# Kernel optimization log

Measured on AMD Instinct MI355X. Metric: run time of the kernel, lower is better.

The kernel has to match this reference:

```python
import jax, jax.numpy as jnp
import numpy as np
from jax import lax

UP = 2
K = 3
IN_C, OUT_C = 64, 64
PAD = K // 2  # 1
WEIGHT_GAIN = 1.0 / np.sqrt(IN_C * K * K)
ACT_GAIN = np.sqrt(2.0)  # lrelu def_gain
CLAMP = 256.0
LRELU_ALPHA = 0.2


def setup_inputs() -> dict:
    key = jax.random.key(0)
    k1, k2 = jax.random.split(key)
    x = jax.random.normal(k1, (16, IN_C, 128, 128), dtype=jnp.float32)
    weight = jax.random.normal(k2, (OUT_C, IN_C, K, K), dtype=jnp.float32)
    bias = jnp.zeros((OUT_C,), dtype=jnp.float32)
    # upfirdn2d.setup_filter((1,3,3,1)): outer product, normalized to sum 1
    a = jnp.array([1.0, 3.0, 3.0, 1.0], dtype=jnp.float32)
    f = jnp.outer(a, a)
    f = f / jnp.sum(f)  # 4x4 separable FIR filter
    return {"x": x, "weight": weight, "bias": bias, "f": f}


def _upfirdn2d_up2(x, f):
    # zero-insertion upsample by 2 + pad + FIR filter, gain = up**2
    N, C, H, W = x.shape
    fw = f.shape[-1]  # 4
    # conv2d_resample padding adjustment for up>1 on top of base padding k//2
    p0 = PAD + (fw + UP - 1) // 2  # 3
    p1 = PAD + (fw - UP) // 2      # 2
    fk = jnp.tile((f * (UP * UP))[None, None], (C, 1, 1, 1))  # [C,1,4,4] depthwise
    # lhs_dilation=2 gives 2H-1 samples; add (UP-1) extra right/bottom zeros to
    # match upfirdn's 2H zero-inserted signal.
    return lax.conv_general_dilated(
        x, fk, window_strides=(1, 1),
        padding=((p0, p1 + UP - 1), (p0, p1 + UP - 1)),
        lhs_dilation=(UP, UP),
        feature_group_count=C,
        dimension_numbers=("NCHW", "OIHW", "NCHW"))


def reference(x, weight, bias, f):
    h = _upfirdn2d_up2(x, f)  # [N, C, 2H+2, 2W+2]
    # conv: flip_weight = (up == 1) = False -> true convolution (flip kernel)
    w = (weight * WEIGHT_GAIN)[:, :, ::-1, ::-1]
    y = lax.conv_general_dilated(
        h, w, window_strides=(1, 1), padding="VALID",
        dimension_numbers=("NCHW", "OIHW", "NCHW"))  # [N, OUT_C, 2H, 2W]
    # fused bias + lrelu + gain + clamp (bias_act with gain=1)
    y = y + bias[None, :, None, None]
    y = jnp.where(y >= 0, y, LRELU_ALPHA * y) * ACT_GAIN
    y = jnp.clip(y, -CLAMP, CLAMP)
    return y
```

## Files before the change

kernel.cpp:

```cpp
#include <hip/hip_runtime.h>

typedef float f32x16 __attribute__((ext_vector_type(16)));
typedef float f32x4  __attribute__((ext_vector_type(4)));
typedef float f32x2  __attribute__((ext_vector_type(2)));
typedef short bf16x8 __attribute__((ext_vector_type(8)));

#define NB 16
#define CI 64
#define CO 64
#define Hh 128
#define Ww 128

__device__ short g_A[9 * 4 * 8 * 64 * 8];
__device__ short g_xh[(size_t)NB * Hh * Ww * CI];

__device__ inline short f2bf(float f) {
  union { float f; unsigned u; } v; v.f = f;
  unsigned r = (v.u + 0x7FFF + ((v.u >> 16) & 1)) >> 16;
  return (short)r;
}

__global__ __launch_bounds__(256) void build_filters(const float* __restrict__ w) {
  const int ef = blockIdx.x * 256 + threadIdx.x;
  if (ef >= 147456) return;
  const int e   = ef & 7;
  const int l   = (ef >> 3) & 63;
  const int mg  = (ef >> 9) & 7;
  const int ks  = (ef >> 12) & 3;
  const int tap = ef >> 14;
  const int r   = l & 31;
  const int px  = r & 1;
  const int py  = mg >> 2;
  const int oc  = (mg & 3) * 16 + (r >> 1);
  const int ic  = ks * 16 + (l >> 5) * 8 + e;
  const int dyi = tap / 3, dxi = tap % 3;
  const int my = 2 * dyi + 1 - py;
  const int mx = 2 * dxi + 1 - px;
  const float FF[4] = {0.25f, 0.75f, 0.75f, 0.25f};
  const float* wp = w + (oc * CI + ic) * 9;
  float s = 0.f;
  #pragma unroll
  for (int ky = 0; ky < 3; ++ky) {
    const int iy = my - ky;
    if (iy < 0 || iy > 3) continue;
    #pragma unroll
    for (int kx = 0; kx < 3; ++kx) {
      const int ix = mx - kx;
      if (ix < 0 || ix > 3) continue;
      s += wp[(2 - ky) * 3 + (2 - kx)] * (FF[iy] * FF[ix]);
    }
  }
  g_A[ef] = f2bf(s * (1.0f / 24.0f));
}

__global__ __launch_bounds__(256) void to_nhwc(const float* __restrict__ x) {
  __shared__ alignas(16) char xt[64 * 512];
  const int b = blockIdx.x;
  const int n = b >> 7, y = b & 127;
  const int tid = threadIdx.x;
  #pragma unroll
  for (int it = 0; it < 8; ++it) {
    const int idx = tid + it * 256;
    const int ic = idx >> 5, xq = idx & 31;
    const f32x4 v = *(const f32x4*)(x + (((size_t)n * CI + ic) * Hh + y) * Ww + xq * 4);
    *(f32x4*)(xt + ic * 512 + ((xq * 16) ^ (((ic >> 3) & 7) * 16))) = v;
  }
  __syncthreads();
  #pragma unroll
  for (int it = 0; it < 4; ++it) {
    const int idx = tid + it * 256;
    const int icb = idx & 7, xp = idx >> 3;
    bf16x8 o;
    #pragma unroll
    for (int j = 0; j < 8; ++j) {
      const int ic = icb * 8 + j;
      const float f = *(const float*)(xt + ic * 512 + (((xp >> 2) * 16) ^ (icb * 16)) + (xp & 3) * 4);
      o[j] = f2bf(f);
    }
    *(bf16x8*)(g_xh + (((size_t)n * Hh + y) * Ww + xp) * CI + icb * 8) = o;
  }
}

#define CH_STR 2896

__global__ __launch_bounds__(256, 2) void mfma_conv(const float* __restrict__ bias,
                                                    float* __restrict__ out) {
  __shared__ alignas(16) char xs[8 * CH_STR];

  const int tid = threadIdx.x;
  const int l   = tid & 63;
  const int wid = tid >> 6;
  const int wm  = wid >> 1;
  const int wn  = wid & 1;
  const int n   = blockIdx.y;
  const int ty0 = blockIdx.x >> 3, tx0 = blockIdx.x & 7;
  const int qb  = ty0 * 8, pb = tx0 * 16;

  bf16x8 a[4][4];
  #pragma unroll
  for (int ks = 0; ks < 4; ++ks)
    #pragma unroll
    for (int mf = 0; mf < 4; ++mf)
      a[ks][mf] = *(const bf16x8*)(g_A + ((ks * 8 + wm * 4 + mf) * 512) + l * 8);

  const size_t xbase = (size_t)n * (Hh * Ww * CI);
  for (int u = tid; u < 1440; u += 256) {
    const int icb8 = u & 7, pix = u >> 3;
    const int yy = pix / 18, xx = pix - yy * 18;
    const int gy = qb - 1 + yy, gx = pb - 1 + xx;
    bf16x8 v = {};
    if ((unsigned)gy < (unsigned)Hh && (unsigned)gx < (unsigned)Ww)
      v = *(const bf16x8*)(g_xh + xbase + (size_t)(gy * Ww + gx) * CI + icb8 * 8);
    *(bf16x8*)(xs + icb8 * CH_STR + pix * 16) = v;
  }
  __syncthreads();

  f32x16 acc[4][2];
  #pragma unroll
  for (int mf = 0; mf < 4; ++mf)
    #pragma unroll
    for (int nf = 0; nf < 2; ++nf)
      #pragma unroll
      for (int r = 0; r < 16; ++r) acc[mf][nf][r] = 0.f;

  const int col = l & 31, kg2 = l >> 5;
  const int p = col & 15, qh = col >> 4;
  int bbase[2];
  #pragma unroll
  for (int nf = 0; nf < 2; ++nf)
    bbase[nf] = kg2 * CH_STR + ((wn * 4 + nf * 2 + qh) * 18 + p) * 16;

  #pragma unroll
  for (int tap = 0; tap < 9; ++tap) {
    const int dyi = tap / 3, dxi = tap % 3;
    const int bsh = (dyi * 18 + dxi) * 16;
    #pragma unroll
    for (int ks = 0; ks < 4; ++ks) {
      bf16x8 b[2];
      #pragma unroll
      for (int nf = 0; nf < 2; ++nf)
        b[nf] = *(const bf16x8*)(xs + bbase[nf] + ks * (2 * CH_STR) + bsh);
      __builtin_amdgcn_s_setprio(1);
      #pragma unroll
      for (int mf = 0; mf < 4; ++mf)
        #pragma unroll
        for (int nf = 0; nf < 2; ++nf)
          acc[mf][nf] = __builtin_amdgcn_mfma_f32_32x32x16_bf16(a[ks][mf], b[nf], acc[mf][nf], 0, 0, 0);
      __builtin_amdgcn_s_setprio(0);
      if (tap < 8) {
        #pragma unroll
        for (int mf = 0; mf < 4; ++mf)
          a[ks][mf] = *(const bf16x8*)(g_A + (((tap + 1) * 4 + ks) * 8 + wm * 4 + mf) * 512 + l * 8);
      }
    }
  }

  float* outp = out + ((size_t)(n * CO) << 16);
  #pragma unroll
  for (int mf = 0; mf < 4; ++mf) {
    #pragma unroll
    for (int nf = 0; nf < 2; ++nf) {
      const int q = wn * 4 + nf * 2 + qh;
      const int y = 2 * (qb + q) + wm;
      const int xd = 2 * (pb + p);
      #pragma unroll
      for (int rp = 0; rp < 8; ++rp) {
        const int oc = mf * 16 + (rp & 1) + 4 * (rp >> 1) + 2 * kg2;
        const float bj = bias[oc];
        float v0 = acc[mf][nf][2 * rp]     + bj;
        float v1 = acc[mf][nf][2 * rp + 1] + bj;
        v0 = (v0 >= 0.f ? v0 : 0.2f * v0) * 1.4142135623730951f;
        v1 = (v1 >= 0.f ? v1 : 0.2f * v1) * 1.4142135623730951f;
        v0 = fminf(256.f, fmaxf(-256.f, v0));
        v1 = fminf(256.f, fmaxf(-256.f, v1));
        f32x2 o; o[0] = v0; o[1] = v1;
        __builtin_nontemporal_store(o, (f32x2*)(outp + ((size_t)oc << 16) + y * 256 + xd));
      }
    }
  }
}

extern "C" void kernel_launch(void* const* d_in, const int* in_sizes, int n_in,
                              void* d_out, int out_size, void* d_ws, size_t ws_size,
                              hipStream_t stream) {
  const float* x    = (const float*)d_in[0];
  const float* w    = (const float*)d_in[1];
  const float* bias = (const float*)d_in[2];
  float* out = (float*)d_out;

  build_filters<<<576, 256, 0, stream>>>(w);
  to_nhwc<<<2048, 256, 0, stream>>>(x);
  mfma_conv<<<dim3(128, NB), 256, 0, stream>>>(bias, out);
}
```

Measured before the change: 115.5 us.

## Merge prep kernels and halve conv tile height for higher occupancy

Folds the filter-building and NHWC-conversion kernels into one launch, with extra blocks handling the weights. The conv kernel's tile shrinks from 8 to 4 low-res rows, each wave now owning all pixels of its 2 M-fragments. The grid doubles, accumulator and A registers halve, LDS shrinks, and launch bounds ask for 3 blocks per SM. The cost is more halo reloading per output and less reuse of A fragments across pixels.

```diff
diff --git a/kernel.cpp b/kernel.cpp
--- a/kernel.cpp
+++ b/kernel.cpp
@@ -20,44 +20,48 @@
   return (short)r;
 }
 
-__global__ __launch_bounds__(256) void build_filters(const float* __restrict__ w) {
-  const int ef = blockIdx.x * 256 + threadIdx.x;
-  if (ef >= 147456) return;
-  const int e   = ef & 7;
-  const int l   = (ef >> 3) & 63;
-  const int mg  = (ef >> 9) & 7;
-  const int ks  = (ef >> 12) & 3;
-  const int tap = ef >> 14;
-  const int r   = l & 31;
-  const int px  = r & 1;
-  const int py  = mg >> 2;
-  const int oc  = (mg & 3) * 16 + (r >> 1);
-  const int ic  = ks * 16 + (l >> 5) * 8 + e;
-  const int dyi = tap / 3, dxi = tap % 3;
-  const int my = 2 * dyi + 1 - py;
-  const int mx = 2 * dxi + 1 - px;
-  const float FF[4] = {0.25f, 0.75f, 0.75f, 0.25f};
-  const float* wp = w + (oc * CI + ic) * 9;
-  float s = 0.f;
-  #pragma unroll
-  for (int ky = 0; ky < 3; ++ky) {
-    const int iy = my - ky;
-    if (iy < 0 || iy > 3) continue;
+__global__ __launch_bounds__(256) void prep(const float* __restrict__ x,
+                                            const float* __restrict__ w) {
+  const int tid = threadIdx.x;
+  if (blockIdx.x >= 2048) {
+    const int base = (blockIdx.x - 2048) * 2304;
     #pragma unroll
-    for (int kx = 0; kx < 3; ++kx) {
-      const int ix = mx - kx;
-      if (ix < 0 || ix > 3) continue;
-      s += wp[(2 - ky) * 3 + (2 - kx)] * (FF[iy] * FF[ix]);
+    for (int i = 0; i < 9; ++i) {
+      const int ef = base + i * 256 + tid;
+      const int e   = ef & 7;
+      const int l   = (ef >> 3) & 63;
+      const int mg  = (ef >> 9) & 7;
+      const int ks  = (ef >> 12) & 3;
+      const int tap = ef >> 14;
+      const int r   = l & 31;
+      const int px  = r & 1;
+      const int py  = mg >> 2;
+      const int oc  = (mg & 3) * 16 + (r >> 1);
+      const int ic  = ks * 16 + (l >> 5) * 8 + e;
+      const int dyi = tap / 3, dxi = tap % 3;
+      const int my = 2 * dyi + 1 - py;
+      const int mx = 2 * dxi + 1 - px;
+      const float FF[4] = {0.25f, 0.75f, 0.75f, 0.25f};
+      const float* wp = w + (oc * CI + ic) * 9;
+      float s = 0.f;
+      #pragma unroll
+      for (int ky = 0; ky < 3; ++ky) {
+        const int iy = my - ky;
+        if (iy < 0 || iy > 3) continue;
+        #pragma unroll
+        for (int kx = 0; kx < 3; ++kx) {
+          const int ix = mx - kx;
+          if (ix < 0 || ix > 3) continue;
+          s += wp[(2 - ky) * 3 + (2 - kx)] * (FF[iy] * FF[ix]);
+        }
+      }
+      g_A[ef] = f2bf(s * (1.0f / 24.0f));
     }
+    return;
   }
-  g_A[ef] = f2bf(s * (1.0f / 24.0f));
-}
-
-__global__ __launch_bounds__(256) void to_nhwc(const float* __restrict__ x) {
   __shared__ alignas(16) char xt[64 * 512];
   const int b = blockIdx.x;
   const int n = b >> 7, y = b & 127;
-  const int tid = threadIdx.x;
   #pragma unroll
   for (int it = 0; it < 8; ++it) {
     const int idx = tid + it * 256;
@@ -81,30 +85,28 @@
   }
 }
 
-#define CH_STR 2896
+#define CH_STR 1728
 
-__global__ __launch_bounds__(256, 2) void mfma_conv(const float* __restrict__ bias,
+__global__ __launch_bounds__(256, 3) void mfma_conv(const float* __restrict__ bias,
                                                     float* __restrict__ out) {
   __shared__ alignas(16) char xs[8 * CH_STR];
 
   const int tid = threadIdx.x;
   const int l   = tid & 63;
   const int wid = tid >> 6;
-  const int wm  = wid >> 1;
-  const int wn  = wid & 1;
   const int n   = blockIdx.y;
   const int ty0 = blockIdx.x >> 3, tx0 = blockIdx.x & 7;
-  const int qb  = ty0 * 8, pb = tx0 * 16;
+  const int qb  = ty0 * 4, pb = tx0 * 16;
 
-  bf16x8 a[4][4];
+  bf16x8 a[4][2];
   #pragma unroll
   for (int ks = 0; ks < 4; ++ks)
     #pragma unroll
-    for (int mf = 0; mf < 4; ++mf)
-      a[ks][mf] = *(const bf16x8*)(g_A + ((ks * 8 + wm * 4 + mf) * 512) + l * 8);
+    for (int mf = 0; mf < 2; ++mf)
+      a[ks][mf] = *(const bf16x8*)(g_A + (ks * 8 + wid * 2 + mf) * 512 + l * 8);
 
   const size_t xbase = (size_t)n * (Hh * Ww * CI);
-  for (int u = tid; u < 1440; u += 256) {
+  for (int u = tid; u < 864; u += 256) {
     const int icb8 = u & 7, pix = u >> 3;
     const int yy = pix / 18, xx = pix - yy * 18;
     const int gy = qb - 1 + yy, gx = pb - 1 + xx;
@@ -115,9 +117,9 @@
   }
   __syncthreads();
 
-  f32x16 acc[4][2];
+  f32x16 acc[2][2];
   #pragma unroll
-  for (int mf = 0; mf < 4; ++mf)
+  for (int mf = 0; mf < 2; ++mf)
     #pragma unroll
     for (int nf = 0; nf < 2; ++nf)
       #pragma unroll
@@ -128,7 +130,7 @@
   int bbase[2];
   #pragma unroll
   for (int nf = 0; nf < 2; ++nf)
-    bbase[nf] = kg2 * CH_STR + ((wn * 4 + nf * 2 + qh) * 18 + p) * 16;
+    bbase[nf] = kg2 * CH_STR + ((nf * 2 + qh) * 18 + p) * 16;
 
   #pragma unroll
   for (int tap = 0; tap < 9; ++tap) {
@@ -142,30 +144,32 @@
         b[nf] = *(const bf16x8*)(xs + bbase[nf] + ks * (2 * CH_STR) + bsh);
       __builtin_amdgcn_s_setprio(1);
       #pragma unroll
-      for (int mf = 0; mf < 4; ++mf)
+      for (int mf = 0; mf < 2; ++mf)
         #pragma unroll
         for (int nf = 0; nf < 2; ++nf)
           acc[mf][nf] = __builtin_amdgcn_mfma_f32_32x32x16_bf16(a[ks][mf], b[nf], acc[mf][nf], 0, 0, 0);
       __builtin_amdgcn_s_setprio(0);
       if (tap < 8) {
         #pragma unroll
-        for (int mf = 0; mf < 4; ++mf)
-          a[ks][mf] = *(const bf16x8*)(g_A + (((tap + 1) * 4 + ks) * 8 + wm * 4 + mf) * 512 + l * 8);
+        for (int mf = 0; mf < 2; ++mf)
+          a[ks][mf] = *(const bf16x8*)(g_A + (((tap + 1) * 4 + ks) * 8 + wid * 2 + mf) * 512 + l * 8);
       }
     }
   }
 
   float* outp = out + ((size_t)(n * CO) << 16);
   #pragma unroll
-  for (int mf = 0; mf < 4; ++mf) {
+  for (int mf = 0; mf < 2; ++mf) {
+    const int mg = wid * 2 + mf;
+    const int py = mg >> 2, och = mg & 3;
     #pragma unroll
     for (int nf = 0; nf < 2; ++nf) {
-      const int q = wn * 4 + nf * 2 + qh;
-      const int y = 2 * (qb + q) + wm;
+      const int q = nf * 2 + qh;
+      const int y = 2 * (qb + q) + py;
       const int xd = 2 * (pb + p);
       #pragma unroll
       for (int rp = 0; rp < 8; ++rp) {
-        const int oc = mf * 16 + (rp & 1) + 4 * (rp >> 1) + 2 * kg2;
+        const int oc = och * 16 + (rp & 1) + 4 * (rp >> 1) + 2 * kg2;
         const float bj = bias[oc];
         float v0 = acc[mf][nf][2 * rp]     + bj;
         float v1 = acc[mf][nf][2 * rp + 1] + bj;
@@ -188,7 +192,6 @@
   const float* bias = (const float*)d_in[2];
   float* out = (float*)d_out;
 
-  build_filters<<<576, 256, 0, stream>>>(w);
-  to_nhwc<<<2048, 256, 0, stream>>>(x);
-  mfma_conv<<<dim3(128, NB), 256, 0, stream>>>(bias, out);
+  prep<<<2112, 256, 0, stream>>>(x, w);
+  mfma_conv<<<dim3(256, NB), 256, 0, stream>>>(bias, out);
 }
```

New measurement: 121.6 us. 1.05x slower.

## Fuse NCHW-to-bf16 conversion into conv kernel via LDS staging

Applied to the files above, without the earlier changes.

Removes the separate to_nhwc kernel and its global bf16 NHWC buffer. The conv kernel now loads the fp32 NCHW halo tile directly into LDS in two 32-channel halves, converts it to bf16, and writes the channel-interleaved layout the MFMA loop expects. The output index mapping is also changed to a py/och decomposition, and the nontemporal stores become regular stores. This saves one launch and a round trip through global memory. In exchange it adds extra LDS, two more barriers and redundant halo reads per block, and the fp32 loads use only 8-byte vectors.

```diff
diff --git a/kernel.cpp b/kernel.cpp
--- a/kernel.cpp
+++ b/kernel.cpp
@@ -12,7 +12,6 @@
 #define Ww 128
 
 __device__ short g_A[9 * 4 * 8 * 64 * 8];
-__device__ short g_xh[(size_t)NB * Hh * Ww * CI];
 
 __device__ inline short f2bf(float f) {
   union { float f; unsigned u; } v; v.f = f;
@@ -53,39 +52,13 @@
   g_A[ef] = f2bf(s * (1.0f / 24.0f));
 }
 
-__global__ __launch_bounds__(256) void to_nhwc(const float* __restrict__ x) {
-  __shared__ alignas(16) char xt[64 * 512];
-  const int b = blockIdx.x;
-  const int n = b >> 7, y = b & 127;
-  const int tid = threadIdx.x;
-  #pragma unroll
-  for (int it = 0; it < 8; ++it) {
-    const int idx = tid + it * 256;
-    const int ic = idx >> 5, xq = idx & 31;
-    const f32x4 v = *(const f32x4*)(x + (((size_t)n * CI + ic) * Hh + y) * Ww + xq * 4);
-    *(f32x4*)(xt + ic * 512 + ((xq * 16) ^ (((ic >> 3) & 7) * 16))) = v;
-  }
-  __syncthreads();
-  #pragma unroll
-  for (int it = 0; it < 4; ++it) {
-    const int idx = tid + it * 256;
-    const int icb = idx & 7, xp = idx >> 3;
-    bf16x8 o;
-    #pragma unroll
-    for (int j = 0; j < 8; ++j) {
-      const int ic = icb * 8 + j;
-      const float f = *(const float*)(xt + ic * 512 + (((xp >> 2) * 16) ^ (icb * 16)) + (xp & 3) * 4);
-      o[j] = f2bf(f);
-    }
-    *(bf16x8*)(g_xh + (((size_t)n * Hh + y) * Ww + xp) * CI + icb * 8) = o;
-  }
-}
-
 #define CH_STR 2896
 
-__global__ __launch_bounds__(256, 2) void mfma_conv(const float* __restrict__ bias,
+__global__ __launch_bounds__(256, 2) void mfma_conv(const float* __restrict__ x,
+                                                    const float* __restrict__ bias,
                                                     float* __restrict__ out) {
   __shared__ alignas(16) char xs[8 * CH_STR];
+  __shared__ alignas(16) float xf[32 * 10 * 20];
 
   const int tid = threadIdx.x;
   const int l   = tid & 63;
@@ -101,19 +74,37 @@
   for (int ks = 0; ks < 4; ++ks)
     #pragma unroll
     for (int mf = 0; mf < 4; ++mf)
-      a[ks][mf] = *(const bf16x8*)(g_A + ((ks * 8 + wm * 4 + mf) * 512) + l * 8);
+      a[ks][mf] = *(const bf16x8*)(g_A + (ks * 8 + wm * 4 + mf) * 512 + l * 8);
 
-  const size_t xbase = (size_t)n * (Hh * Ww * CI);
-  for (int u = tid; u < 1440; u += 256) {
-    const int icb8 = u & 7, pix = u >> 3;
-    const int yy = pix / 18, xx = pix - yy * 18;
-    const int gy = qb - 1 + yy, gx = pb - 1 + xx;
-    bf16x8 v = {};
-    if ((unsigned)gy < (unsigned)Hh && (unsigned)gx < (unsigned)Ww)
-      v = *(const bf16x8*)(g_xh + xbase + (size_t)(gy * Ww + gx) * CI + icb8 * 8);
-    *(bf16x8*)(xs + icb8 * CH_STR + pix * 16) = v;
+  const float* xn = x + (size_t)n * (CI * Hh * Ww);
+  #pragma unroll
+  for (int c = 0; c < 2; ++c) {
+    for (int v = tid; v < 3200; v += 256) {
+      const int col2  = v % 10;
+      const int rowic = v / 10;
+      const int row   = rowic % 10;
+      const int icl   = rowic / 10;
+      const int gy = qb - 1 + row;
+      const int gx = pb - 2 + 2 * col2;
+      f32x2 p2 = {};
+      if ((unsigned)gy < (unsigned)Hh && (unsigned)gx < (unsigned)Ww)
+        p2 = *(const f32x2*)(xn + ((size_t)(c * 32 + icl) * Hh + gy) * Ww + gx);
+      *(f32x2*)(xf + (icl * 10 + row) * 20 + 2 * col2) = p2;
+    }
+    __syncthreads();
+    for (int u = tid; u < 720; u += 256) {
+      const int pix  = u % 180;
+      const int icb2 = u / 180;
+      const int row = pix / 18, xx = pix - row * 18;
+      const float* src = xf + row * 20 + (xx + 1);
+      bf16x8 o;
+      #pragma unroll
+      for (int j = 0; j < 8; ++j)
+        o[j] = f2bf(src[(icb2 * 8 + j) * 200]);
+      *(bf16x8*)(xs + (c * 4 + icb2) * CH_STR + pix * 16) = o;
+    }
+    __syncthreads();
   }
-  __syncthreads();
 
   f32x16 acc[4][2];
   #pragma unroll
@@ -158,14 +149,16 @@
   float* outp = out + ((size_t)(n * CO) << 16);
   #pragma unroll
   for (int mf = 0; mf < 4; ++mf) {
+    const int mg = wm * 4 + mf;
+    const int py = mg >> 2, och = mg & 3;
     #pragma unroll
     for (int nf = 0; nf < 2; ++nf) {
       const int q = wn * 4 + nf * 2 + qh;
-      const int y = 2 * (qb + q) + wm;
+      const int y = 2 * (qb + q) + py;
       const int xd = 2 * (pb + p);
       #pragma unroll
       for (int rp = 0; rp < 8; ++rp) {
-        const int oc = mf * 16 + (rp & 1) + 4 * (rp >> 1) + 2 * kg2;
+        const int oc = och * 16 + (rp & 1) + 4 * (rp >> 1) + 2 * kg2;
         const float bj = bias[oc];
         float v0 = acc[mf][nf][2 * rp]     + bj;
         float v1 = acc[mf][nf][2 * rp + 1] + bj;
@@ -174,7 +167,7 @@
         v0 = fminf(256.f, fmaxf(-256.f, v0));
         v1 = fminf(256.f, fmaxf(-256.f, v1));
         f32x2 o; o[0] = v0; o[1] = v1;
-        __builtin_nontemporal_store(o, (f32x2*)(outp + ((size_t)oc << 16) + y * 256 + xd));
+        *(f32x2*)(outp + ((size_t)oc << 16) + y * 256 + xd) = o;
       }
     }
   }
@@ -189,6 +182,5 @@
   float* out = (float*)d_out;
 
   build_filters<<<576, 256, 0, stream>>>(w);
-  to_nhwc<<<2048, 256, 0, stream>>>(x);
-  mfma_conv<<<dim3(128, NB), 256, 0, stream>>>(bias, out);
+  mfma_conv<<<dim3(128, NB), 256, 0, stream>>>(x, bias, out);
 }
```

Measured after the change: 139.6 us. 1.21x slower.

## Retile conv blocks to wide 4x64 input strips split by output-row parity

Applied to the files above, without the earlier changes.

Each block of the fused conv kernel now covers a 4-row by 64-column input strip and only one output-row parity, instead of an 8x16 strip with both parities. Each warp now holds 2 output-channel fragments and 4 pixel fragments rather than 4 and 2. The aim is longer contiguous output-row segments per store, for better write coalescing on the large fp32 output, and a different A/B fragment reuse balance. In exchange, each input tile is staged twice (once per parity) with a larger halo, and shared memory per block grows to about 50 KB.

```diff
diff --git a/kernel.cpp b/kernel.cpp
--- a/kernel.cpp
+++ b/kernel.cpp
@@ -81,11 +81,11 @@
   }
 }
 
-#define CH_STR 2896
+#define CH 6352
 
 __global__ __launch_bounds__(256, 2) void mfma_conv(const float* __restrict__ bias,
                                                     float* __restrict__ out) {
-  __shared__ alignas(16) char xs[8 * CH_STR];
+  __shared__ alignas(16) char xs[8 * CH];
 
   const int tid = threadIdx.x;
   const int l   = tid & 63;
@@ -93,79 +93,84 @@
   const int wm  = wid >> 1;
   const int wn  = wid & 1;
   const int n   = blockIdx.y;
-  const int ty0 = blockIdx.x >> 3, tx0 = blockIdx.x & 7;
-  const int qb  = ty0 * 8, pb = tx0 * 16;
+  const int zs  = blockIdx.x & 1;
+  const int pt  = (blockIdx.x >> 1) & 1;
+  const int qt  = blockIdx.x >> 2;
+  const int qb  = qt * 4, pb = pt * 64;
 
-  bf16x8 a[4][4];
+  bf16x8 a[4][2];
   #pragma unroll
   for (int ks = 0; ks < 4; ++ks)
     #pragma unroll
-    for (int mf = 0; mf < 4; ++mf)
-      a[ks][mf] = *(const bf16x8*)(g_A + ((ks * 8 + wm * 4 + mf) * 512) + l * 8);
+    for (int mf = 0; mf < 2; ++mf)
+      a[ks][mf] = *(const bf16x8*)(g_A + (ks * 8 + zs * 4 + wm * 2 + mf) * 512 + l * 8);
 
   const size_t xbase = (size_t)n * (Hh * Ww * CI);
-  for (int u = tid; u < 1440; u += 256) {
+  for (int u = tid; u < 3168; u += 256) {
     const int icb8 = u & 7, pix = u >> 3;
-    const int yy = pix / 18, xx = pix - yy * 18;
+    const int yy = pix / 66, xx = pix - yy * 66;
     const int gy = qb - 1 + yy, gx = pb - 1 + xx;
     bf16x8 v = {};
     if ((unsigned)gy < (unsigned)Hh && (unsigned)gx < (unsigned)Ww)
       v = *(const bf16x8*)(g_xh + xbase + (size_t)(gy * Ww + gx) * CI + icb8 * 8);
-    *(bf16x8*)(xs + icb8 * CH_STR + pix * 16) = v;
+    *(bf16x8*)(xs + icb8 * CH + pix * 16) = v;
   }
   __syncthreads();
 
-  f32x16 acc[4][2];
+  f32x16 acc[2][4];
   #pragma unroll
-  for (int mf = 0; mf < 4; ++mf)
+  for (int mf = 0; mf < 2; ++mf)
     #pragma unroll
-    for (int nf = 0; nf < 2; ++nf)
+    for (int nf = 0; nf < 4; ++nf)
       #pragma unroll
       for (int r = 0; r < 16; ++r) acc[mf][nf][r] = 0.f;
 
   const int col = l & 31, kg2 = l >> 5;
-  const int p = col & 15, qh = col >> 4;
-  int bbase[2];
+  int bbase[4];
   #pragma unroll
-  for (int nf = 0; nf < 2; ++nf)
-    bbase[nf] = kg2 * CH_STR + ((wn * 4 + nf * 2 + qh) * 18 + p) * 16;
+  for (int nf = 0; nf < 4; ++nf) {
+    const int q = wn * 2 + (nf >> 1);
+    const int p = (nf & 1) * 32 + col;
+    bbase[nf] = kg2 * CH + (q * 66 + p) * 16;
+  }
 
   #pragma unroll
   for (int tap = 0; tap < 9; ++tap) {
     const int dyi = tap / 3, dxi = tap % 3;
-    const int bsh = (dyi * 18 + dxi) * 16;
+    const int bsh = (dyi * 66 + dxi) * 16;
     #pragma unroll
     for (int ks = 0; ks < 4; ++ks) {
-      bf16x8 b[2];
+      bf16x8 b[4];
       #pragma unroll
-      for (int nf = 0; nf < 2; ++nf)
-        b[nf] = *(const bf16x8*)(xs + bbase[nf] + ks * (2 * CH_STR) + bsh);
+      for (int nf = 0; nf < 4; ++nf)
+        b[nf] = *(const bf16x8*)(xs + bbase[nf] + ks * (2 * CH) + bsh);
       __builtin_amdgcn_s_setprio(1);
       #pragma unroll
-      for (int mf = 0; mf < 4; ++mf)
+      for (int mf = 0; mf < 2; ++mf)
         #pragma unroll
-        for (int nf = 0; nf < 2; ++nf)
+        for (int nf = 0; nf < 4; ++nf)
           acc[mf][nf] = __builtin_amdgcn_mfma_f32_32x32x16_bf16(a[ks][mf], b[nf], acc[mf][nf], 0, 0, 0);
       __builtin_amdgcn_s_setprio(0);
       if (tap < 8) {
         #pragma unroll
-        for (int mf = 0; mf < 4; ++mf)
-          a[ks][mf] = *(const bf16x8*)(g_A + (((tap + 1) * 4 + ks) * 8 + wm * 4 + mf) * 512 + l * 8);
+        for (int mf = 0; mf < 2; ++mf)
+          a[ks][mf] = *(const bf16x8*)(g_A + (((tap + 1) * 4 + ks) * 8 + zs * 4 + wm * 2 + mf) * 512 + l * 8);
       }
     }
   }
 
   float* outp = out + ((size_t)(n * CO) << 16);
   #pragma unroll
-  for (int mf = 0; mf < 4; ++mf) {
+  for (int mf = 0; mf < 2; ++mf) {
+    const int och = wm * 2 + mf;
     #pragma unroll
-    for (int nf = 0; nf < 2; ++nf) {
-      const int q = wn * 4 + nf * 2 + qh;
-      const int y = 2 * (qb + q) + wm;
-      const int xd = 2 * (pb + p);
+    for (int nf = 0; nf < 4; ++nf) {
+      const int q = wn * 2 + (nf >> 1);
+      const int y = 2 * (qb + q) + zs;
+      const int xd = 2 * (pb + (nf & 1) * 32 + col);
       #pragma unroll
       for (int rp = 0; rp < 8; ++rp) {
-        const int oc = mf * 16 + (rp & 1) + 4 * (rp >> 1) + 2 * kg2;
+        const int oc = och * 16 + (rp & 1) + 4 * (rp >> 1) + 2 * kg2;
         const float bj = bias[oc];
         float v0 = acc[mf][nf][2 * rp]     + bj;
         float v1 = acc[mf][nf][2 * rp + 1] + bj;
```

After: 125.3 us. +8.5%, slower.
